# Kernel tuning notes

Hardware: AMD Instinct MI355X
Metric: run time of the kernel (lower is better)

The kernel has to match this reference:

```python
import jax, jax.numpy as jnp
import numpy as np

N_IN = 200000   # active input voxels
N_OUT = 200000  # stride-1 submanifold conv: out_nnz == in_nnz
K_VOL = 27      # 3x3x3 kernel volume
M = 100000      # gathered pairs per kernel offset
C_IN = 64
C_OUT = 64


def setup_inputs() -> dict:
    key = jax.random.key(0)
    k1, k2, k3, k4, k5 = jax.random.split(key, 5)
    in_feats = jax.random.normal(k1, (N_IN, C_IN), dtype=jnp.float32)
    kernel = jax.random.normal(k2, (K_VOL, C_IN, C_OUT), dtype=jnp.float32) * (1.0 / np.sqrt(C_IN))
    bias = jax.random.normal(k3, (C_OUT,), dtype=jnp.float32)
    imap = jax.random.randint(k4, (K_VOL, M), 0, N_IN, dtype=jnp.int32)
    omap = jax.random.randint(k5, (K_VOL, M), 0, N_OUT, dtype=jnp.int32)
    return {"in_feats": in_feats, "kernel": kernel, "bias": bias,
            "imap": imap, "omap": omap}


def reference(in_feats, kernel, bias, imap, omap):
    # Sparse 3D conv: per-kernel-offset gather -> GEMM -> scatter-add.
    # gathered: [K_VOL, M, C_IN]
    gathered = in_feats[imap]
    # per-offset GEMM: [K_VOL, M, C_OUT]
    contrib = jnp.einsum('kmc,kco->kmo', gathered, kernel)
    # scatter-add into output rows: [N_OUT, C_OUT]
    out = jnp.zeros((N_OUT, C_OUT), dtype=in_feats.dtype)
    out = out.at[omap].add(contrib)
    return out + bias
```

## Files before the change

### kernel.cpp

```cpp
#include <hip/hip_runtime.h>
#include <hip/hip_fp16.h>

#define N_IN 200000
#define N_OUT 200000
#define K_VOL 27
#define M_PAIRS 100000
#define C_IN 64
#define C_OUT 64
#define NPAIRS (K_VOL * M_PAIRS)

#define MTILE 64
#define LDS_PAD 72

typedef __attribute__((ext_vector_type(4))) float floatx4;
typedef __attribute__((ext_vector_type(8))) short shortx8;
typedef __attribute__((ext_vector_type(8))) _Float16 halfx8;
typedef __attribute__((ext_vector_type(2))) _Float16 half2v;

#define FEATS_OFF   0UL
#define FEATS_BYTES (200000UL * 64 * 2)
#define WT_OFF      (FEATS_OFF + FEATS_BYTES)
#define WT_BYTES    (27UL * 64 * 64 * 2)
#define ACC_OFF     ((WT_OFF + WT_BYTES + 255UL) & ~255UL)
#define ACC_BYTES   (200000UL * 64 * 2)
#define WS_NEEDED   (ACC_OFF + ACC_BYTES)
#define WS_FALLBACK (WT_OFF + WT_BYTES)

static __device__ __forceinline__ ushort f32_to_f16_bits(float f) {
    union { _Float16 h; ushort u; } cv;
    cv.h = (_Float16)f;
    return cv.u;
}

static __device__ __forceinline__ void atomic_pk_add_f16(ushort* addr, float lo, float hi) {
    half2v v;
    v[0] = (_Float16)lo;
    v[1] = (_Float16)hi;
#if defined(__has_builtin) && __has_builtin(__builtin_amdgcn_global_atomic_fadd_v2f16)
    typedef half2v __attribute__((address_space(1))) *as1p;
    __builtin_amdgcn_global_atomic_fadd_v2f16((as1p)(unsigned long long)addr, v);
#else
    unsafeAtomicAdd((__half2*)addr, *(__half2*)&v);
#endif
}

__global__ void cvt_feats_kernel(const float* __restrict__ src, ushort* __restrict__ dst, int n4) {
    int i = blockIdx.x * blockDim.x + threadIdx.x;
    if (i >= n4) return;
    float4 v = ((const float4*)src)[i];
    ushort4 o;
    o.x = f32_to_f16_bits(v.x); o.y = f32_to_f16_bits(v.y);
    o.z = f32_to_f16_bits(v.z); o.w = f32_to_f16_bits(v.w);
    ((ushort4*)dst)[i] = o;
}

__global__ void cvt_wt_kernel(const float* __restrict__ w, ushort* __restrict__ wt) {
    int idx = blockIdx.x * blockDim.x + threadIdx.x;
    if (idx >= K_VOL * C_IN * C_OUT) return;
    int k   = idx >> 12;
    int rem = idx & 4095;
    int c   = rem >> 6;
    int o   = rem & 63;
    wt[(k << 12) + (o << 6) + c] = f32_to_f16_bits(w[idx]);
}

__launch_bounds__(256, 4)
__global__ void spconv_f16_kernel(const ushort* __restrict__ feats,
                                  const ushort* __restrict__ wt,
                                  const int* __restrict__ imap,
                                  const int* __restrict__ omap,
                                  ushort* __restrict__ accum) {
    __shared__ ushort Asm[MTILE * LDS_PAD];
    __shared__ ushort Wsm[C_OUT * LDS_PAD];
    __shared__ int omap_s[MTILE];

    const int k   = blockIdx.y;
    const int m0  = blockIdx.x * MTILE;
    const int tid = threadIdx.x;
    const int kM  = k * M_PAIRS;

    #pragma unroll
    for (int p = 0; p < 2; ++p) {
        int cid = tid + p * 256;
        int row = cid >> 3;
        int ch  = cid & 7;
        *(shortx8*)&Wsm[row * LDS_PAD + ch * 8] =
            *(const shortx8*)&wt[(k << 12) + row * 64 + ch * 8];
    }
    #pragma unroll
    for (int p = 0; p < 2; ++p) {
        int cid = tid + p * 256;
        int row = cid >> 3;
        int ch  = cid & 7;
        int m   = m0 + row;
        shortx8 v = {0, 0, 0, 0, 0, 0, 0, 0};
        if (m < M_PAIRS) {
            int g = imap[kM + m];
            v = *(const shortx8*)&feats[(g << 6) + ch * 8];
        }
        *(shortx8*)&Asm[row * LDS_PAD + ch * 8] = v;
    }
    if (tid < MTILE) {
        int m = m0 + tid;
        omap_s[tid] = (m < M_PAIRS) ? omap[kM + m] : -1;
    }
    __syncthreads();

    const int wave = tid >> 6;
    const int lane = tid & 63;
    const int quad = lane >> 4;
    const int l16  = lane & 15;
    const int rbase = wave * 16;
    const bool even = (l16 & 1) == 0;

    const halfx8 a0 = *(const halfx8*)&Asm[(rbase + l16) * LDS_PAD + quad * 8];
    const halfx8 a1 = *(const halfx8*)&Asm[(rbase + l16) * LDS_PAD + 32 + quad * 8];

    #pragma unroll
    for (int ct = 0; ct < 4; ++ct) {
        const halfx8 b0 = *(const halfx8*)&Wsm[(ct * 16 + l16) * LDS_PAD + quad * 8];
        const halfx8 b1 = *(const halfx8*)&Wsm[(ct * 16 + l16) * LDS_PAD + 32 + quad * 8];
        floatx4 acc = {0.f, 0.f, 0.f, 0.f};
        acc = __builtin_amdgcn_mfma_f32_16x16x32_f16(a0, b0, acc, 0, 0, 0);
        acc = __builtin_amdgcn_mfma_f32_16x16x32_f16(a1, b1, acc, 0, 0, 0);

        float p0 = __shfl_xor(acc[0], 1, 64);
        float p1 = __shfl_xor(acc[1], 1, 64);
        float p2 = __shfl_xor(acc[2], 1, 64);
        float p3 = __shfl_xor(acc[3], 1, 64);

        const int colb = ct * 16 + (l16 & ~1);
        float lo0, hi0, lo1, hi1;
        int r0;
        if (even) { r0 = 0; lo0 = acc[0]; hi0 = p0; lo1 = acc[1]; hi1 = p1; }
        else      { r0 = 2; lo0 = p2;     hi0 = acc[2]; lo1 = p3; hi1 = acc[3]; }

        int row0 = rbase + quad * 4 + r0;
        int o0 = omap_s[row0];
        int o1 = omap_s[row0 + 1];
        if (o0 >= 0) atomic_pk_add_f16(&accum[(o0 << 6) + colb], lo0, hi0);
        if (o1 >= 0) atomic_pk_add_f16(&accum[(o1 << 6) + colb], lo1, hi1);
    }
}

__global__ void finalize_kernel(const ushort* __restrict__ accum,
                                const float* __restrict__ bias,
                                float* __restrict__ out, int n8) {
    int i = blockIdx.x * blockDim.x + threadIdx.x;
    if (i >= n8) return;
    halfx8 h = *(const halfx8*)&accum[(size_t)i * 8];
    int c = (i * 8) & 63;
    float4 b0 = *(const float4*)(bias + c);
    float4 b1 = *(const float4*)(bias + c + 4);
    float4 o0, o1;
    o0.x = (float)h[0] + b0.x; o0.y = (float)h[1] + b0.y;
    o0.z = (float)h[2] + b0.z; o0.w = (float)h[3] + b0.w;
    o1.x = (float)h[4] + b1.x; o1.y = (float)h[5] + b1.y;
    o1.z = (float)h[6] + b1.z; o1.w = (float)h[7] + b1.w;
    ((float4*)out)[(size_t)i * 2]     = o0;
    ((float4*)out)[(size_t)i * 2 + 1] = o1;
}

__global__ void init_bias_kernel(const float* __restrict__ bias, float* __restrict__ out, int n4) {
    int i = blockIdx.x * blockDim.x + threadIdx.x;
    if (i >= n4) return;
    int c = (i * 4) & 63;
    float4 b = *(const float4*)(bias + c);
    ((float4*)out)[i] = b;
}

__launch_bounds__(256, 4)
__global__ void spconv_push_f32_kernel(const ushort* __restrict__ feats,
                                       const ushort* __restrict__ wt,
                                       const int* __restrict__ imap,
                                       const int* __restrict__ omap,
                                       float* __restrict__ out) {
    __shared__ ushort Asm[MTILE * LDS_PAD];
    __shared__ ushort Wsm[C_OUT * LDS_PAD];
    __shared__ int omap_s[MTILE];

    const int k   = blockIdx.y;
    const int m0  = blockIdx.x * MTILE;
    const int tid = threadIdx.x;
    const int kM  = k * M_PAIRS;

    #pragma unroll
    for (int p = 0; p < 2; ++p) {
        int cid = tid + p * 256;
        int row = cid >> 3;
        int ch  = cid & 7;
        *(shortx8*)&Wsm[row * LDS_PAD + ch * 8] =
            *(const shortx8*)&wt[(k << 12) + row * 64 + ch * 8];
    }
    #pragma unroll
    for (int p = 0; p < 2; ++p) {
        int cid = tid + p * 256;
        int row = cid >> 3;
        int ch  = cid & 7;
        int m   = m0 + row;
        shortx8 v = {0, 0, 0, 0, 0, 0, 0, 0};
        if (m < M_PAIRS) {
            int g = imap[kM + m];
            v = *(const shortx8*)&feats[(g << 6) + ch * 8];
        }
        *(shortx8*)&Asm[row * LDS_PAD + ch * 8] = v;
    }
    if (tid < MTILE) {
        int m = m0 + tid;
        omap_s[tid] = (m < M_PAIRS) ? omap[kM + m] : -1;
    }
    __syncthreads();

    const int wave = tid >> 6;
    const int lane = tid & 63;
    const int quad = lane >> 4;
    const int l16  = lane & 15;
    const int rbase = wave * 16;

    const halfx8 a0 = *(const halfx8*)&Asm[(rbase + l16) * LDS_PAD + quad * 8];
    const halfx8 a1 = *(const halfx8*)&Asm[(rbase + l16) * LDS_PAD + 32 + quad * 8];

    #pragma unroll
    for (int ct = 0; ct < 4; ++ct) {
        const halfx8 b0 = *(const halfx8*)&Wsm[(ct * 16 + l16) * LDS_PAD + quad * 8];
        const halfx8 b1 = *(const halfx8*)&Wsm[(ct * 16 + l16) * LDS_PAD + 32 + quad * 8];
        floatx4 acc = {0.f, 0.f, 0.f, 0.f};
        acc = __builtin_amdgcn_mfma_f32_16x16x32_f16(a0, b0, acc, 0, 0, 0);
        acc = __builtin_amdgcn_mfma_f32_16x16x32_f16(a1, b1, acc, 0, 0, 0);
        const int col = ct * 16 + l16;
        #pragma unroll
        for (int r = 0; r < 4; ++r) {
            int rl = rbase + quad * 4 + r;
            int orow = omap_s[rl];
            if (orow >= 0) atomicAdd(&out[(orow << 6) + col], acc[r]);
        }
    }
}

extern "C" void kernel_launch(void* const* d_in, const int* in_sizes, int n_in,
                              void* d_out, int out_size, void* d_ws, size_t ws_size,
                              hipStream_t stream) {
    const float* in_feats = (const float*)d_in[0];
    const float* kernelw  = (const float*)d_in[1];
    const float* bias     = (const float*)d_in[2];
    const int*   imap     = (const int*)d_in[3];
    const int*   omap     = (const int*)d_in[4];
    float* out = (float*)d_out;

    char* ws = (char*)d_ws;
    ushort* feats_h = (ushort*)(ws + FEATS_OFF);
    ushort* wt_h    = (ushort*)(ws + WT_OFF);

    int n4 = N_IN * C_IN / 4;
    cvt_feats_kernel<<<(n4 + 255) / 256, 256, 0, stream>>>(in_feats, feats_h, n4);
    cvt_wt_kernel<<<(K_VOL * C_IN * C_OUT + 255) / 256, 256, 0, stream>>>(kernelw, wt_h);

    dim3 grid((M_PAIRS + MTILE - 1) / MTILE, K_VOL);

    if (ws_size >= WS_NEEDED) {
        ushort* accum = (ushort*)(ws + ACC_OFF);
        hipMemsetAsync(accum, 0, ACC_BYTES, stream);
        spconv_f16_kernel<<<grid, 256, 0, stream>>>(feats_h, wt_h, imap, omap, accum);
        int n8 = N_OUT * C_OUT / 8;
        finalize_kernel<<<(n8 + 255) / 256, 256, 0, stream>>>(accum, bias, out, n8);
    } else {
        int o4 = N_OUT * C_OUT / 4;
        init_bias_kernel<<<(o4 + 255) / 256, 256, 0, stream>>>(bias, out, o4);
        spconv_push_f32_kernel<<<grid, 256, 0, stream>>>(feats_h, wt_h, imap, omap, out);
    }
}
```

Measured before the change: 667.3 us.

## Replace global atomic scatter with bucket-sorted pull accumulation per output tile

Builds a counting sort of the gather/scatter pairs by (output tile, kernel offset) using histogram, three-stage scan and fill kernels. A new pull kernel assigns one block per 64-row output tile, loops over kernel offsets and accumulates the MFMA results into a shared-memory fp32 tile with LDS atomics, then adds bias and writes the output directly. This removes the fp16 global atomics, the accumulator memset and the finalize pass. In exchange it adds sorting passes with their own global atomics, and it cuts per-block parallelism with partially filled MFMA tiles.

```diff
diff --git a/kernel.cpp b/kernel.cpp
--- a/kernel.cpp
+++ b/kernel.cpp
@@ -9,39 +9,35 @@
 #define C_OUT 64
 #define NPAIRS (K_VOL * M_PAIRS)
 
-#define MTILE 64
+#define NTILES (N_OUT / 64)
+#define NBUCKETS (NTILES * K_VOL)
+#define SCAN_NB1 330
+
 #define LDS_PAD 72
+#define OT_PAD 68
 
 typedef __attribute__((ext_vector_type(4))) float floatx4;
 typedef __attribute__((ext_vector_type(8))) short shortx8;
 typedef __attribute__((ext_vector_type(8))) _Float16 halfx8;
-typedef __attribute__((ext_vector_type(2))) _Float16 half2v;
 
 #define FEATS_OFF   0UL
 #define FEATS_BYTES (200000UL * 64 * 2)
 #define WT_OFF      (FEATS_OFF + FEATS_BYTES)
 #define WT_BYTES    (27UL * 64 * 64 * 2)
-#define ACC_OFF     ((WT_OFF + WT_BYTES + 255UL) & ~255UL)
-#define ACC_BYTES   (200000UL * 64 * 2)
-#define WS_NEEDED   (ACC_OFF + ACC_BYTES)
-#define WS_FALLBACK (WT_OFF + WT_BYTES)
+#define OFFS_OFF    ((WT_OFF + WT_BYTES + 255UL) & ~255UL)
+#define OFFS_BYTES  (337920UL)
+#define CNT_OFF     (OFFS_OFF + OFFS_BYTES)
+#define CNT_BYTES   (337920UL)
+#define BSUM_OFF    (CNT_OFF + CNT_BYTES)
+#define BSUM_BYTES  (2048UL)
+#define SORT_OFF    (BSUM_OFF + BSUM_BYTES)
+#define SORT_BYTES  (2700000UL * 4)
+#define WS_NEEDED   (SORT_OFF + SORT_BYTES)
 
 static __device__ __forceinline__ ushort f32_to_f16_bits(float f) {
     union { _Float16 h; ushort u; } cv;
     cv.h = (_Float16)f;
     return cv.u;
-}
-
-static __device__ __forceinline__ void atomic_pk_add_f16(ushort* addr, float lo, float hi) {
-    half2v v;
-    v[0] = (_Float16)lo;
-    v[1] = (_Float16)hi;
-#if defined(__has_builtin) && __has_builtin(__builtin_amdgcn_global_atomic_fadd_v2f16)
-    typedef half2v __attribute__((address_space(1))) *as1p;
-    __builtin_amdgcn_global_atomic_fadd_v2f16((as1p)(unsigned long long)addr, v);
-#else
-    unsafeAtomicAdd((__half2*)addr, *(__half2*)&v);
-#endif
 }
 
 __global__ void cvt_feats_kernel(const float* __restrict__ src, ushort* __restrict__ dst, int n4) {
@@ -64,18 +60,185 @@
     wt[(k << 12) + (o << 6) + c] = f32_to_f16_bits(w[idx]);
 }
 
+__global__ void hist_kernel(const int* __restrict__ omap, int* __restrict__ counts) {
+    int p = blockIdx.x * blockDim.x + threadIdx.x;
+    if (p >= NPAIRS) return;
+    int k = p / M_PAIRS;
+    int o = omap[p];
+    atomicAdd(&counts[(o >> 6) * K_VOL + k], 1);
+}
+
+__global__ void scan1_kernel(const int* __restrict__ counts, int* __restrict__ bsum) {
+    __shared__ int sd[256];
+    int tid = threadIdx.x;
+    int i = blockIdx.x * 256 + tid;
+    sd[tid] = (i < NBUCKETS) ? counts[i] : 0;
+    __syncthreads();
+    for (int s = 128; s > 0; s >>= 1) {
+        if (tid < s) sd[tid] += sd[tid + s];
+        __syncthreads();
+    }
+    if (tid == 0) bsum[blockIdx.x] = sd[0];
+}
+
+__global__ void scan2_kernel(int* __restrict__ bsum) {
+    __shared__ int sd[512];
+    int tid = threadIdx.x;
+    int v = (tid < SCAN_NB1) ? bsum[tid] : 0;
+    sd[tid] = v;
+    __syncthreads();
+    for (int off = 1; off < 512; off <<= 1) {
+        int t = (tid >= off) ? sd[tid - off] : 0;
+        __syncthreads();
+        sd[tid] += t;
+        __syncthreads();
+    }
+    if (tid < SCAN_NB1) bsum[tid] = sd[tid] - v;
+}
+
+__global__ void scan3_kernel(int* __restrict__ counts_cursor, const int* __restrict__ bsum,
+                             int* __restrict__ offsets) {
+    __shared__ int sd[256];
+    int tid = threadIdx.x;
+    int i = blockIdx.x * 256 + tid;
+    int v = (i < NBUCKETS) ? counts_cursor[i] : 0;
+    sd[tid] = v;
+    __syncthreads();
+    for (int off = 1; off < 256; off <<= 1) {
+        int t = (tid >= off) ? sd[tid - off] : 0;
+        __syncthreads();
+        sd[tid] += t;
+        __syncthreads();
+    }
+    int excl = sd[tid] - v + bsum[blockIdx.x];
+    if (i <= NBUCKETS) offsets[i] = excl;
+    if (i < NBUCKETS) counts_cursor[i] = excl;
+}
+
+__global__ void fill_kernel(const int* __restrict__ imap, const int* __restrict__ omap,
+                            int* __restrict__ cursor, int* __restrict__ sorted_arr) {
+    int p = blockIdx.x * blockDim.x + threadIdx.x;
+    if (p >= NPAIRS) return;
+    int k = p / M_PAIRS;
+    int o = omap[p];
+    int slot = atomicAdd(&cursor[(o >> 6) * K_VOL + k], 1);
+    sorted_arr[slot] = (imap[p] & 0x3FFFF) | ((o & 63) << 18);
+}
+
 __launch_bounds__(256, 4)
-__global__ void spconv_f16_kernel(const ushort* __restrict__ feats,
-                                  const ushort* __restrict__ wt,
-                                  const int* __restrict__ imap,
-                                  const int* __restrict__ omap,
-                                  ushort* __restrict__ accum) {
-    __shared__ ushort Asm[MTILE * LDS_PAD];
-    __shared__ ushort Wsm[C_OUT * LDS_PAD];
-    __shared__ int omap_s[MTILE];
+__global__ void spconv_pull_kernel(const ushort* __restrict__ feats,
+                                   const ushort* __restrict__ wt,
+                                   const int* __restrict__ offsets,
+                                   const int* __restrict__ sorted_arr,
+                                   const float* __restrict__ bias,
+                                   float* __restrict__ out) {
+    __shared__ ushort Asm[64 * LDS_PAD];
+    __shared__ ushort Wsm[64 * LDS_PAD];
+    __shared__ float  out_t[65 * OT_PAD];
+    __shared__ int    olist[64];
+
+    const int otile = blockIdx.x;
+    const int tid   = threadIdx.x;
+    const int base  = otile * K_VOL;
+
+    for (int i = tid; i < 65 * OT_PAD; i += 256) out_t[i] = 0.f;
+
+    const int wave = tid >> 6;
+    const int lane = tid & 63;
+    const int quad = lane >> 4;
+    const int l16  = lane & 15;
+
+    for (int k = 0; k < K_VOL; ++k) {
+        int beg = offsets[base + k];
+        int end = offsets[base + k + 1];
+        if (beg == end) continue;
+
+        __syncthreads();
+        #pragma unroll
+        for (int p = 0; p < 2; ++p) {
+            int cid = tid + p * 256;
+            int row = cid >> 3;
+            int ch  = cid & 7;
+            *(shortx8*)&Wsm[row * LDS_PAD + ch * 8] =
+                *(const shortx8*)&wt[(k << 12) + row * 64 + ch * 8];
+        }
+        __syncthreads();
+
+        const halfx8 b0 = *(const halfx8*)&Wsm[(wave * 16 + l16) * LDS_PAD + quad * 8];
+        const halfx8 b1 = *(const halfx8*)&Wsm[(wave * 16 + l16) * LDS_PAD + 32 + quad * 8];
+
+        for (int pos = beg; pos < end; pos += 64) {
+            int g = end - pos; if (g > 64) g = 64;
+
+            __syncthreads();
+            #pragma unroll
+            for (int p = 0; p < 2; ++p) {
+                int cid = tid + p * 256;
+                int row = cid >> 3;
+                int ch  = cid & 7;
+                shortx8 v = {0, 0, 0, 0, 0, 0, 0, 0};
+                if (row < g) {
+                    int rec = sorted_arr[pos + row];
+                    int in_row = rec & 0x3FFFF;
+                    v = *(const shortx8*)&feats[((size_t)in_row << 6) + ch * 8];
+                }
+                *(shortx8*)&Asm[row * LDS_PAD + ch * 8] = v;
+            }
+            if (tid < 64)
+                olist[tid] = (tid < g) ? ((sorted_arr[pos + tid] >> 18) & 63) : 64;
+            __syncthreads();
+
+            int nsc = (g + 15) >> 4;
+            for (int sc = 0; sc < nsc; ++sc) {
+                const halfx8 a0 = *(const halfx8*)&Asm[(sc * 16 + l16) * LDS_PAD + quad * 8];
+                const halfx8 a1 = *(const halfx8*)&Asm[(sc * 16 + l16) * LDS_PAD + 32 + quad * 8];
+                floatx4 acc = {0.f, 0.f, 0.f, 0.f};
+                acc = __builtin_amdgcn_mfma_f32_16x16x32_f16(a0, b0, acc, 0, 0, 0);
+                acc = __builtin_amdgcn_mfma_f32_16x16x32_f16(a1, b1, acc, 0, 0, 0);
+                const int col = wave * 16 + l16;
+                const int rb  = sc * 16 + quad * 4;
+                #pragma unroll
+                for (int r = 0; r < 4; ++r) {
+                    int ol = olist[rb + r];
+                    atomicAdd(&out_t[ol * OT_PAD + col], acc[r]);
+                }
+            }
+        }
+    }
+
+    __syncthreads();
+    #pragma unroll
+    for (int p = 0; p < 4; ++p) {
+        int cid = tid + p * 256;
+        int row = cid >> 4;
+        int ch  = cid & 15;
+        float4 v = *(float4*)&out_t[row * OT_PAD + ch * 4];
+        float4 b = ((const float4*)bias)[ch];
+        v.x += b.x; v.y += b.y; v.z += b.z; v.w += b.w;
+        ((float4*)out)[(size_t)(otile * 64 + row) * 16 + ch] = v;
+    }
+}
+
+__global__ void init_bias_kernel(const float* __restrict__ bias, float* __restrict__ out, int n4) {
+    int i = blockIdx.x * blockDim.x + threadIdx.x;
+    if (i >= n4) return;
+    int c = (i * 4) & 63;
+    float4 b = *(const float4*)(bias + c);
+    ((float4*)out)[i] = b;
+}
+
+__launch_bounds__(256, 4)
+__global__ void spconv_push_f32_kernel(const ushort* __restrict__ feats,
+                                       const ushort* __restrict__ wt,
+                                       const int* __restrict__ imap,
+                                       const int* __restrict__ omap,
+                                       float* __restrict__ out) {
+    __shared__ ushort Asm[64 * LDS_PAD];
+    __shared__ ushort Wsm[64 * LDS_PAD];
+    __shared__ int omap_s[64];
 
     const int k   = blockIdx.y;
-    const int m0  = blockIdx.x * MTILE;
+    const int m0  = blockIdx.x * 64;
     const int tid = threadIdx.x;
     const int kM  = k * M_PAIRS;
 
@@ -100,112 +263,7 @@
         }
         *(shortx8*)&Asm[row * LDS_PAD + ch * 8] = v;
     }
-    if (tid < MTILE) {
-        int m = m0 + tid;
-        omap_s[tid] = (m < M_PAIRS) ? omap[kM + m] : -1;
-    }
-    __syncthreads();
-
-    const int wave = tid >> 6;
-    const int lane = tid & 63;
-    const int quad = lane >> 4;
-    const int l16  = lane & 15;
-    const int rbase = wave * 16;
-    const bool even = (l16 & 1) == 0;
-
-    const halfx8 a0 = *(const halfx8*)&Asm[(rbase + l16) * LDS_PAD + quad * 8];
-    const halfx8 a1 = *(const halfx8*)&Asm[(rbase + l16) * LDS_PAD + 32 + quad * 8];
-
-    #pragma unroll
-    for (int ct = 0; ct < 4; ++ct) {
-        const halfx8 b0 = *(const halfx8*)&Wsm[(ct * 16 + l16) * LDS_PAD + quad * 8];
-        const halfx8 b1 = *(const halfx8*)&Wsm[(ct * 16 + l16) * LDS_PAD + 32 + quad * 8];
-        floatx4 acc = {0.f, 0.f, 0.f, 0.f};
-        acc = __builtin_amdgcn_mfma_f32_16x16x32_f16(a0, b0, acc, 0, 0, 0);
-        acc = __builtin_amdgcn_mfma_f32_16x16x32_f16(a1, b1, acc, 0, 0, 0);
-
-        float p0 = __shfl_xor(acc[0], 1, 64);
-        float p1 = __shfl_xor(acc[1], 1, 64);
-        float p2 = __shfl_xor(acc[2], 1, 64);
-        float p3 = __shfl_xor(acc[3], 1, 64);
-
-        const int colb = ct * 16 + (l16 & ~1);
-        float lo0, hi0, lo1, hi1;
-        int r0;
-        if (even) { r0 = 0; lo0 = acc[0]; hi0 = p0; lo1 = acc[1]; hi1 = p1; }
-        else      { r0 = 2; lo0 = p2;     hi0 = acc[2]; lo1 = p3; hi1 = acc[3]; }
-
-        int row0 = rbase + quad * 4 + r0;
-        int o0 = omap_s[row0];
-        int o1 = omap_s[row0 + 1];
-        if (o0 >= 0) atomic_pk_add_f16(&accum[(o0 << 6) + colb], lo0, hi0);
-        if (o1 >= 0) atomic_pk_add_f16(&accum[(o1 << 6) + colb], lo1, hi1);
-    }
-}
-
-__global__ void finalize_kernel(const ushort* __restrict__ accum,
-                                const float* __restrict__ bias,
-                                float* __restrict__ out, int n8) {
-    int i = blockIdx.x * blockDim.x + threadIdx.x;
-    if (i >= n8) return;
-    halfx8 h = *(const halfx8*)&accum[(size_t)i * 8];
-    int c = (i * 8) & 63;
-    float4 b0 = *(const float4*)(bias + c);
-    float4 b1 = *(const float4*)(bias + c + 4);
-    float4 o0, o1;
-    o0.x = (float)h[0] + b0.x; o0.y = (float)h[1] + b0.y;
-    o0.z = (float)h[2] + b0.z; o0.w = (float)h[3] + b0.w;
-    o1.x = (float)h[4] + b1.x; o1.y = (float)h[5] + b1.y;
-    o1.z = (float)h[6] + b1.z; o1.w = (float)h[7] + b1.w;
-    ((float4*)out)[(size_t)i * 2]     = o0;
-    ((float4*)out)[(size_t)i * 2 + 1] = o1;
-}
-
-__global__ void init_bias_kernel(const float* __restrict__ bias, float* __restrict__ out, int n4) {
-    int i = blockIdx.x * blockDim.x + threadIdx.x;
-    if (i >= n4) return;
-    int c = (i * 4) & 63;
-    float4 b = *(const float4*)(bias + c);
-    ((float4*)out)[i] = b;
-}
-
-__launch_bounds__(256, 4)
-__global__ void spconv_push_f32_kernel(const ushort* __restrict__ feats,
-                                       const ushort* __restrict__ wt,
-                                       const int* __restrict__ imap,
-                                       const int* __restrict__ omap,
-                                       float* __restrict__ out) {
-    __shared__ ushort Asm[MTILE * LDS_PAD];
-    __shared__ ushort Wsm[C_OUT * LDS_PAD];
-    __shared__ int omap_s[MTILE];
-
-    const int k   = blockIdx.y;
-    const int m0  = blockIdx.x * MTILE;
-    const int tid = threadIdx.x;
-    const int kM  = k * M_PAIRS;
-
-    #pragma unroll
-    for (int p = 0; p < 2; ++p) {
-        int cid = tid + p * 256;
-        int row = cid >> 3;
-        int ch  = cid & 7;
-        *(shortx8*)&Wsm[row * LDS_PAD + ch * 8] =
-            *(const shortx8*)&wt[(k << 12) + row * 64 + ch * 8];
-    }
-    #pragma unroll
-    for (int p = 0; p < 2; ++p) {
-        int cid = tid + p * 256;
-        int row = cid >> 3;
-        int ch  = cid & 7;
-        int m   = m0 + row;
-        shortx8 v = {0, 0, 0, 0, 0, 0, 0, 0};
-        if (m < M_PAIRS) {
-            int g = imap[kM + m];
-            v = *(const shortx8*)&feats[(g << 6) + ch * 8];
-        }
-        *(shortx8*)&Asm[row * LDS_PAD + ch * 8] = v;
-    }
-    if (tid < MTILE) {
+    if (tid < 64) {
         int m = m0 + tid;
         omap_s[tid] = (m < M_PAIRS) ? omap[kM + m] : -1;
     }
@@ -255,17 +313,24 @@
     cvt_feats_kernel<<<(n4 + 255) / 256, 256, 0, stream>>>(in_feats, feats_h, n4);
     cvt_wt_kernel<<<(K_VOL * C_IN * C_OUT + 255) / 256, 256, 0, stream>>>(kernelw, wt_h);
 
-    dim3 grid((M_PAIRS + MTILE - 1) / MTILE, K_VOL);
-
     if (ws_size >= WS_NEEDED) {
-        ushort* accum = (ushort*)(ws + ACC_OFF);
-        hipMemsetAsync(accum, 0, ACC_BYTES, stream);
-        spconv_f16_kernel<<<grid, 256, 0, stream>>>(feats_h, wt_h, imap, omap, accum);
-        int n8 = N_OUT * C_OUT / 8;
-        finalize_kernel<<<(n8 + 255) / 256, 256, 0, stream>>>(accum, bias, out, n8);
+        int* offsets = (int*)(ws + OFFS_OFF);
+        int* counts  = (int*)(ws + CNT_OFF);
+        int* bsum    = (int*)(ws + BSUM_OFF);
+        int* sorted_arr = (int*)(ws + SORT_OFF);
+
+        hipMemsetAsync(counts, 0, NBUCKETS * sizeof(int), stream);
+        hist_kernel<<<(NPAIRS + 255) / 256, 256, 0, stream>>>(omap, counts);
+        scan1_kernel<<<SCAN_NB1, 256, 0, stream>>>(counts, bsum);
+        scan2_kernel<<<1, 512, 0, stream>>>(bsum);
+        scan3_kernel<<<SCAN_NB1, 256, 0, stream>>>(counts, bsum, offsets);
+        fill_kernel<<<(NPAIRS + 255) / 256, 256, 0, stream>>>(imap, omap, counts, sorted_arr);
+
+        spconv_pull_kernel<<<NTILES, 256, 0, stream>>>(feats_h, wt_h, offsets, sorted_arr, bias, out);
     } else {
         int o4 = N_OUT * C_OUT / 4;
         init_bias_kernel<<<(o4 + 255) / 256, 256, 0, stream>>>(bias, out, o4);
+        dim3 grid((M_PAIRS + 63) / 64, K_VOL);
         spconv_push_f32_kernel<<<grid, 256, 0, stream>>>(feats_h, wt_h, imap, omap, out);
     }
 }
```

Measured after the change: 1.640 ms. +145.8%, slower.
